# Kernel optimization log

Hardware: AMD Instinct MI355X
Metric: run time of the kernel (lower is better)

The kernel has to match this reference:

```python
import jax, jax.numpy as jnp
import numpy as np

T, B, C = 2048, 8, 1024
H, K, P = 16, 31, 15  # num_heads, kernel_size, padding_l
R = C // H


def setup_inputs() -> dict:
    key = jax.random.key(0)
    k1, k2 = jax.random.split(key)
    x = jax.random.normal(k1, (T, B, C), dtype=jnp.float32)
    # weight_linear.weight, xavier-ish scale, shape (H*K, C)
    W = jax.random.normal(k2, (H * K, C), dtype=jnp.float32) * (2.0 / (C + H * K)) ** 0.5
    return {"x": x, "W": W}


def reference(x, W):
    # per-position dynamic kernels: (T,B,H,K)
    w = jnp.einsum('tbc,oc->tbo', x, W).reshape(T, B, H, K)
    w = jax.nn.softmax(w, axis=-1)  # weight_softmax=True
    # depthwise dynamic conv: out[t] = sum_k w[t,:,:,k] * x[t - P + k]
    xr = x.reshape(T, B, H, R)
    xp = jnp.pad(xr, ((P, K - 1 - P), (0, 0), (0, 0), (0, 0)))
    out = jnp.zeros_like(xr)
    for k in range(K):  # fixed small kernel-size loop, fuses under jit
        out = out + w[:, :, :, k:k + 1] * jax.lax.dynamic_slice_in_dim(xp, k, T, axis=0)
    return out.reshape(T, B, C)
```

## Files before the change

kernel.cpp:

```cpp
#include <hip/hip_runtime.h>
#include <cstddef>
#include <cstdint>

constexpr int T_ = 2048;
constexpr int B_ = 8;
constexpr int C_ = 1024;
constexpr int H_ = 16;
constexpr int K_ = 31;
constexpr int P_ = 15;
constexpr int M_ = T_ * B_;
constexpr int N_ = H_ * K_;
constexpr int NP = 512;

typedef _Float16 f16x4 __attribute__((ext_vector_type(4)));
typedef _Float16 f16x8 __attribute__((ext_vector_type(8)));
typedef float f32x4 __attribute__((ext_vector_type(4)));

__device__ __forceinline__ void async_cp16(const void* g, void* l) {
    __builtin_amdgcn_global_load_lds(
        (const __attribute__((address_space(1))) void*)g,
        (__attribute__((address_space(3))) void*)l, 16, 0, 0);
}

constexpr int XCH = M_ * C_ / 8;
constexpr int WCH = NP * C_ / 8;

__global__ __launch_bounds__(256)
void cvt_inputs(const float* __restrict__ X, const float* __restrict__ W,
                _Float16* __restrict__ Xh, _Float16* __restrict__ Wh) {
    const int id = blockIdx.x * 256 + threadIdx.x;
    if (id < XCH) {
        const float4 v0 = *(const float4*)(X + (size_t)id * 8);
        const float4 v1 = *(const float4*)(X + (size_t)id * 8 + 4);
        f16x8 hv;
        hv[0] = (_Float16)v0.x; hv[1] = (_Float16)v0.y;
        hv[2] = (_Float16)v0.z; hv[3] = (_Float16)v0.w;
        hv[4] = (_Float16)v1.x; hv[5] = (_Float16)v1.y;
        hv[6] = (_Float16)v1.z; hv[7] = (_Float16)v1.w;
        *(f16x8*)(Xh + (size_t)id * 8) = hv;
    } else {
        const int j = id - XCH;
        const int n = j >> 7, sp = j & 127;
        const int h = n >> 5, k = n & 31;
        f16x8 hv = {};
        if (k < 31) {
            const float* wp = W + (size_t)(h * 31 + k) * C_ + sp * 8;
            const float4 v0 = *(const float4*)(wp);
            const float4 v1 = *(const float4*)(wp + 4);
            hv[0] = (_Float16)v0.x; hv[1] = (_Float16)v0.y;
            hv[2] = (_Float16)v0.z; hv[3] = (_Float16)v0.w;
            hv[4] = (_Float16)v1.x; hv[5] = (_Float16)v1.y;
            hv[6] = (_Float16)v1.z; hv[7] = (_Float16)v1.w;
        }
        *(f16x8*)(Wh + (size_t)n * C_ + sp * 8) = hv;
    }
}

__global__ __launch_bounds__(256)
void gemm_softmax(const _Float16* __restrict__ Xh,
                  const _Float16* __restrict__ Wh,
                  _Float16* __restrict__ WSM) {
    __shared__ union {
        struct { _Float16 A[2][128 * 64]; _Float16 B[2][128 * 64]; } s;
        _Float16 Ls[128 * 136];
    } u;

    const int tid = threadIdx.x;
    const int lane = tid & 63;
    const int w = tid >> 6;
    const int wm = (w >> 1) * 64;
    const int wn = (w & 1) * 64;
    const int col = lane & 15;
    const int g = lane >> 4;
    const int m0 = blockIdx.x * 128;
    const int n0 = blockIdx.y * 128;

    const _Float16* asrc[4];
    const _Float16* bsrc[4];
#pragma unroll
    for (int p = 0; p < 4; ++p) {
        const int ci = p * 256 + tid;
        const int r = ci >> 3, cs = ci & 7;
        const int cl = cs ^ (r & 7);
        asrc[p] = Xh + (size_t)(m0 + r) * C_ + cl * 8;
        bsrc[p] = Wh + (size_t)(n0 + r) * C_ + cl * 8;
    }

    f32x4 acc[4][4] = {};

#pragma unroll
    for (int p = 0; p < 4; ++p) {
        const int ci = p * 256 + tid;
        async_cp16(asrc[p], &u.s.A[0][ci * 8]);
        async_cp16(bsrc[p], &u.s.B[0][ci * 8]);
    }
    __syncthreads();

    int cur = 0;
    for (int t = 0; t < 16; ++t) {
        if (t < 15) {
            const int k1 = (t + 1) * 64;
#pragma unroll
            for (int p = 0; p < 4; ++p) {
                const int ci = p * 256 + tid;
                async_cp16(asrc[p] + k1, &u.s.A[cur ^ 1][ci * 8]);
                async_cp16(bsrc[p] + k1, &u.s.B[cur ^ 1][ci * 8]);
            }
        }

        f16x8 a[2][4], b[2][4];
#pragma unroll
        for (int kk = 0; kk < 2; ++kk) {
#pragma unroll
            for (int mf = 0; mf < 4; ++mf) {
                const int row = wm + mf * 16 + col;
                const int c = ((kk << 2) | g) ^ (row & 7);
                a[kk][mf] = *(const f16x8*)&u.s.A[cur][row * 64 + c * 8];
            }
#pragma unroll
            for (int nf = 0; nf < 4; ++nf) {
                const int row = wn + nf * 16 + col;
                const int c = ((kk << 2) | g) ^ (row & 7);
                b[kk][nf] = *(const f16x8*)&u.s.B[cur][row * 64 + c * 8];
            }
        }
#pragma unroll
        for (int kk = 0; kk < 2; ++kk)
#pragma unroll
            for (int nf = 0; nf < 4; ++nf)
#pragma unroll
                for (int mf = 0; mf < 4; ++mf)
                    acc[mf][nf] = __builtin_amdgcn_mfma_f32_16x16x32_f16(
                        a[kk][mf], b[kk][nf], acc[mf][nf], 0, 0, 0);
        __syncthreads();
        cur ^= 1;
    }

    const int rb = g * 4;
#pragma unroll
    for (int nf = 0; nf < 4; ++nf) {
        const int nl = wn + nf * 16 + col;
#pragma unroll
        for (int mf = 0; mf < 4; ++mf) {
            const int row = wm + mf * 16 + rb;
#pragma unroll
            for (int r = 0; r < 4; ++r)
                u.Ls[(row + r) * 136 + nl] = (_Float16)acc[mf][nf][r];
        }
    }
    __syncthreads();

#pragma unroll
    for (int p = 0; p < 2; ++p) {
        const int task = tid + p * 256;
        const int row = task >> 2, hl = task & 3;
        const _Float16* lp = &u.Ls[row * 136 + hl * 32];
        float v[32];
#pragma unroll
        for (int c = 0; c < 4; ++c) {
            const f16x8 ch = *(const f16x8*)(lp + c * 8);
#pragma unroll
            for (int e = 0; e < 8; ++e) v[c * 8 + e] = (float)ch[e];
        }
        float mx = v[0];
#pragma unroll
        for (int k = 1; k < 31; ++k) mx = fmaxf(mx, v[k]);
        float ssum = 0.f;
#pragma unroll
        for (int k = 0; k < 31; ++k) { v[k] = __expf(v[k] - mx); ssum += v[k]; }
        const float inv = 1.f / ssum;
        _Float16* op = WSM + (size_t)(m0 + row) * NP + n0 + hl * 32;
#pragma unroll
        for (int c = 0; c < 4; ++c) {
            f16x8 ov;
#pragma unroll
            for (int e = 0; e < 8; ++e) {
                const int k = c * 8 + e;
                ov[e] = (k < 31) ? (_Float16)(v[k] * inv) : (_Float16)0.f;
            }
            *(f16x8*)(op + c * 8) = ov;
        }
    }
}

__global__ __launch_bounds__(256)
void dconv(const _Float16* __restrict__ Xh, const _Float16* __restrict__ WSM,
           float* __restrict__ out) {
    __shared__ float xs[94][64];
    __shared__ float ws[64][36];

    const int tid = threadIdx.x;
    const int t0 = blockIdx.x * 64;
    const int bh = (int)blockIdx.y;
    const int b = bh >> 4, h = bh & 15;

    for (int task = tid; task < 94 * 8; task += 256) {
        const int r = task >> 3, hc = task & 7;
        const int tp = t0 + r - 15;
        f16x8 v = {};
        if (tp >= 0 && tp < T_)
            v = *(const f16x8*)(Xh + ((size_t)tp * B_ + b) * C_ + h * 64 + hc * 8);
        f32x4 lo, hi;
        lo[0] = (float)v[0]; lo[1] = (float)v[1];
        lo[2] = (float)v[2]; lo[3] = (float)v[3];
        hi[0] = (float)v[4]; hi[1] = (float)v[5];
        hi[2] = (float)v[6]; hi[3] = (float)v[7];
        const int c0 = (2 * hc) ^ (r & 7), c1 = (2 * hc + 1) ^ (r & 7);
        *(f32x4*)&xs[r][c0 * 4] = lo;
        *(f32x4*)&xs[r][c1 * 4] = hi;
    }
    {
        const int t = tid >> 2, kc = (tid & 3) * 8;
        const f16x8 wv =
            *(const f16x8*)(WSM + ((size_t)(t0 + t) * B_ + b) * NP + h * 32 + kc);
#pragma unroll
        for (int e = 0; e < 8; ++e) ws[t][kc + e] = (float)wv[e];
    }
    __syncthreads();

    const int s = tid & 15;
    const int tg4 = (tid >> 4) * 4;
    f32x4 acc[4] = {};
    f32x4 wc[4];

#pragma unroll
    for (int rr = 0; rr < 34; ++rr) {
        const int r = tg4 + rr;
        const f32x4 xv = *(const f32x4*)&xs[r][(s ^ (r & 7)) * 4];
#pragma unroll
        for (int i = 0; i < 4; ++i) {
            const int k = rr - i;
            if (k < 0 || k > 30) continue;
            if ((k & 3) == 0) wc[i] = *(const f32x4*)&ws[tg4 + i][k];
            acc[i] += wc[i][k & 3] * xv;
        }
    }

#pragma unroll
    for (int i = 0; i < 4; ++i) {
        const int t = t0 + tg4 + i;
        *(f32x4*)(out + ((size_t)t * B_ + b) * C_ + h * 64 + s * 4) = acc[i];
    }
}

extern "C" void kernel_launch(void* const* d_in, const int* in_sizes, int n_in,
                              void* d_out, int out_size, void* d_ws,
                              size_t ws_size, hipStream_t stream) {
    const float* X = (const float*)d_in[0];
    const float* W = (const float*)d_in[1];
    float* out = (float*)d_out;

    _Float16* Wh = (_Float16*)d_ws;
    _Float16* WSM = (_Float16*)((char*)d_ws + (size_t)NP * C_ * 2);
    _Float16* Xh = (_Float16*)((char*)d_ws + (size_t)NP * C_ * 2 +
                               (size_t)M_ * NP * 2);

    cvt_inputs<<<(XCH + WCH) / 256, 256, 0, stream>>>(X, W, Xh, Wh);
    gemm_softmax<<<dim3(M_ / 128, NP / 128), 256, 0, stream>>>(Xh, Wh, WSM);
    dconv<<<dim3(T_ / 64, B_ * H_), 256, 0, stream>>>(Xh, WSM, out);
}
```

Measured before the change: 76.05 us.

## Triple-buffer A tiles with partial vmcnt waits in GEMM; vectorize weight LDS stores

The GEMM mainloop now keeps three A-tile buffers and prefetches A two steps ahead and B one step ahead. The full __syncthreads is replaced by a partial s_waitcnt vmcnt plus a raw barrier, so the next tile's loads can stay in flight across the barrier. The goal is to hide global-load latency better, at the cost of more LDS per block (which may lower occupancy) and fragile manual counter accounting. Separately, the dconv kernel writes the converted softmax weights to LDS as two float4 stores instead of eight scalar stores.

```diff
diff --git a/kernel.cpp b/kernel.cpp
--- a/kernel.cpp
+++ b/kernel.cpp
@@ -61,7 +61,7 @@
                   const _Float16* __restrict__ Wh,
                   _Float16* __restrict__ WSM) {
     __shared__ union {
-        struct { _Float16 A[2][128 * 64]; _Float16 B[2][128 * 64]; } s;
+        struct { _Float16 A[3][128 * 64]; _Float16 B[2][128 * 64]; } s;
         _Float16 Ls[128 * 136];
     } u;
 
@@ -92,19 +92,38 @@
     for (int p = 0; p < 4; ++p) {
         const int ci = p * 256 + tid;
         async_cp16(asrc[p], &u.s.A[0][ci * 8]);
+    }
+#pragma unroll
+    for (int p = 0; p < 4; ++p) {
+        const int ci = p * 256 + tid;
         async_cp16(bsrc[p], &u.s.B[0][ci * 8]);
     }
-    __syncthreads();
-
-    int cur = 0;
+#pragma unroll
+    for (int p = 0; p < 4; ++p) {
+        const int ci = p * 256 + tid;
+        async_cp16(asrc[p] + 64, &u.s.A[1][ci * 8]);
+    }
+    asm volatile("s_waitcnt vmcnt(4)" ::: "memory");
+    __builtin_amdgcn_s_barrier();
+    __builtin_amdgcn_sched_barrier(0);
+
     for (int t = 0; t < 16; ++t) {
+        const int ca = t % 3, cb = t & 1;
         if (t < 15) {
             const int k1 = (t + 1) * 64;
 #pragma unroll
             for (int p = 0; p < 4; ++p) {
                 const int ci = p * 256 + tid;
-                async_cp16(asrc[p] + k1, &u.s.A[cur ^ 1][ci * 8]);
-                async_cp16(bsrc[p] + k1, &u.s.B[cur ^ 1][ci * 8]);
+                async_cp16(bsrc[p] + k1, &u.s.B[cb ^ 1][ci * 8]);
+            }
+        }
+        if (t < 14) {
+            const int k2 = (t + 2) * 64;
+            const int ca2 = (t + 2) % 3;
+#pragma unroll
+            for (int p = 0; p < 4; ++p) {
+                const int ci = p * 256 + tid;
+                async_cp16(asrc[p] + k2, &u.s.A[ca2][ci * 8]);
             }
         }
 
@@ -115,13 +134,13 @@
             for (int mf = 0; mf < 4; ++mf) {
                 const int row = wm + mf * 16 + col;
                 const int c = ((kk << 2) | g) ^ (row & 7);
-                a[kk][mf] = *(const f16x8*)&u.s.A[cur][row * 64 + c * 8];
+                a[kk][mf] = *(const f16x8*)&u.s.A[ca][row * 64 + c * 8];
             }
 #pragma unroll
             for (int nf = 0; nf < 4; ++nf) {
                 const int row = wn + nf * 16 + col;
                 const int c = ((kk << 2) | g) ^ (row & 7);
-                b[kk][nf] = *(const f16x8*)&u.s.B[cur][row * 64 + c * 8];
+                b[kk][nf] = *(const f16x8*)&u.s.B[cb][row * 64 + c * 8];
             }
         }
 #pragma unroll
@@ -132,8 +151,14 @@
                 for (int mf = 0; mf < 4; ++mf)
                     acc[mf][nf] = __builtin_amdgcn_mfma_f32_16x16x32_f16(
                         a[kk][mf], b[kk][nf], acc[mf][nf], 0, 0, 0);
-        __syncthreads();
-        cur ^= 1;
+
+        if (t < 14) {
+            asm volatile("s_waitcnt vmcnt(4)" ::: "memory");
+        } else {
+            asm volatile("s_waitcnt vmcnt(0)" ::: "memory");
+        }
+        __builtin_amdgcn_s_barrier();
+        __builtin_amdgcn_sched_barrier(0);
     }
 
     const int rb = g * 4;
@@ -213,8 +238,13 @@
         const int t = tid >> 2, kc = (tid & 3) * 8;
         const f16x8 wv =
             *(const f16x8*)(WSM + ((size_t)(t0 + t) * B_ + b) * NP + h * 32 + kc);
-#pragma unroll
-        for (int e = 0; e < 8; ++e) ws[t][kc + e] = (float)wv[e];
+        f32x4 lo, hi;
+        lo[0] = (float)wv[0]; lo[1] = (float)wv[1];
+        lo[2] = (float)wv[2]; lo[3] = (float)wv[3];
+        hi[0] = (float)wv[4]; hi[1] = (float)wv[5];
+        hi[2] = (float)wv[6]; hi[3] = (float)wv[7];
+        *(f32x4*)&ws[t][kc] = lo;
+        *(f32x4*)&ws[t][kc + 4] = hi;
     }
     __syncthreads();
 
```

Result: faster. 73.69 us (-3.1%).
